# Kernel optimization log

Measured on AMD Instinct MI355X. Metric: run time of the kernel, lower is better.

Reference implementation:

```python
import jax, jax.numpy as jnp
import numpy as np

RADIUS = 4
SIGMA_1 = 5.0
SIGMA_2 = 1.0


def _gaussian_kernel(dtype):
    # norm.pdf(d)/norm.pdf(0) == exp(-d^2/2)
    x2 = jnp.linspace(-RADIUS, RADIUS, 2 * RADIUS + 1) ** 2
    dist = jnp.sqrt(x2[:, None] + x2[None, :]) / SIGMA_1
    return jnp.exp(-0.5 * dist ** 2).astype(dtype)  # [k, k]


def setup_inputs() -> dict:
    key = jax.random.key(0)
    k1, k2 = jax.random.split(key)
    labels = jax.random.uniform(k1, (16, 20, 256, 256), dtype=jnp.float32)
    inputs = jax.random.uniform(k2, (16, 3, 256, 256), dtype=jnp.float32)
    return {"labels": labels, "inputs": inputs}


def reference(labels, inputs):
    B, K, H, W = labels.shape
    kernel = _gaussian_kernel(labels.dtype)

    # per-class mean color: mean(inputs * probs, HW) / (mean(probs, HW) + 1e-5)
    pmean = jnp.mean(labels, axis=(2, 3))                           # [B, K]
    xmean = jnp.einsum('bchw,bkhw->bkc', inputs, labels) / (H * W)  # [B, K, C]
    class_mean = xmean / (pmean[..., None] + 1e-5)                  # [B, K, C]

    # diff = sum_c (x_c - m_c)^2, expanded to avoid a [B,K,C,H,W] intermediate
    x2sum = jnp.sum(inputs ** 2, axis=1)                            # [B, H, W]
    cross = jnp.einsum('bchw,bkc->bkhw', inputs, class_mean)        # [B, K, H, W]
    m2 = jnp.sum(class_mean ** 2, axis=-1)                          # [B, K]
    diff = x2sum[:, None] - 2.0 * cross + m2[:, :, None, None]      # [B, K, H, W]
    weights = jnp.exp(-(diff ** 2) / (SIGMA_2 ** 2))                # [B, K, H, W]

    def blur(x):  # single-channel gaussian conv, vectorized over B*K
        lhs = x.reshape(B * K, 1, H, W)
        rhs = kernel[None, None]  # [1, 1, k, k]
        y = jax.lax.conv_general_dilated(
            lhs, rhs, window_strides=(1, 1),
            padding=[(RADIUS, RADIUS), (RADIUS, RADIUS)],
            dimension_numbers=('NCHW', 'OIHW', 'NCHW'))
        return y.reshape(B, K, H, W)

    num = jnp.sum(labels * blur(labels * weights), axis=(0, 2, 3))  # [K]
    den = jnp.sum(labels * blur(weights), axis=(0, 2, 3))           # [K]
    loss = jnp.sum(jnp.abs(num / (den + 1e-6)))
    return jnp.asarray(K, labels.dtype) - loss
```

## Files before the change

### kernel.cpp

```cpp
#include <hip/hip_runtime.h>

#define B_ 16
#define K_ 20
#define H_ 256
#define W_ 256
#define HW_ (H_*W_)
#define BK_ (B_*K_)
#define TH_ 64
#define BATCH_ 8
#define KT_ 5
#define SCH_ 16
#define NBLK_FUSED_ (4*K_*B_)

#define WS_ND_   (SCH_*4*BK_)
#define WS_CNT_  (WS_ND_ + 2*NBLK_FUSED_)

#define G1T 0.980198673f
#define G2T 0.923116346f
#define G3T 0.835270211f
#define G4T 0.726149037f

__device__ __forceinline__ float rfl(float v) {
    return __int_as_float(__builtin_amdgcn_readfirstlane(__float_as_int(v)));
}

__global__ __launch_bounds__(256) void stats_k(const float* __restrict__ labels,
                                               const float* __restrict__ inputs,
                                               float* __restrict__ ws) {
    const int x = threadIdx.x;
    const int chunk = blockIdx.x;
    const int kt = blockIdx.y;
    const int b  = blockIdx.z;
    const int k0 = kt * KT_;
    if (chunk == 0 && kt == 0 && b == 0 && x == 0)
        ((unsigned*)(ws + WS_CNT_))[0] = 0u;

    const int cbase = chunk * (16 * W_ / 4);
    const float4* in0 = (const float4*)inputs + (size_t)b * 3 * (HW_/4) + cbase;
    const float4* in1 = in0 + (HW_/4);
    const float4* in2 = in1 + (HW_/4);
    const float4* lb  = (const float4*)labels + (size_t)(b * K_ + k0) * (HW_/4) + cbase;

    float acc[KT_][4];
#pragma unroll
    for (int kk = 0; kk < KT_; ++kk)
        acc[kk][0] = acc[kk][1] = acc[kk][2] = acc[kk][3] = 0.f;

#pragma unroll
    for (int it = 0; it < 4; ++it) {
        const int idx = it * 256 + x;
        const float4 a0 = in0[idx];
        const float4 a1 = in1[idx];
        const float4 a2 = in2[idx];
        float4 lv[KT_];
#pragma unroll
        for (int kk = 0; kk < KT_; ++kk) lv[kk] = lb[kk * (HW_/4) + idx];
#pragma unroll
        for (int kk = 0; kk < KT_; ++kk) {
            const float4 l = lv[kk];
            acc[kk][0] += (l.x + l.y) + (l.z + l.w);
            acc[kk][1] += fmaf(l.w, a0.w, fmaf(l.z, a0.z, fmaf(l.y, a0.y, l.x * a0.x)));
            acc[kk][2] += fmaf(l.w, a1.w, fmaf(l.z, a1.z, fmaf(l.y, a1.y, l.x * a1.x)));
            acc[kk][3] += fmaf(l.w, a2.w, fmaf(l.z, a2.z, fmaf(l.y, a2.y, l.x * a2.x)));
        }
    }

#pragma unroll
    for (int kk = 0; kk < KT_; ++kk)
#pragma unroll
        for (int q = 0; q < 4; ++q)
            for (int o = 32; o > 0; o >>= 1)
                acc[kk][q] += __shfl_down(acc[kk][q], o);

    __shared__ float sred[4][KT_][4];
    const int widx = x >> 6, lane = x & 63;
    if (lane == 0)
#pragma unroll
        for (int kk = 0; kk < KT_; ++kk)
#pragma unroll
            for (int q = 0; q < 4; ++q) sred[widx][kk][q] = acc[kk][q];
    __syncthreads();
    if (x < KT_ * 4) {
        const int kk = x >> 2, q = x & 3;
        const float v = sred[0][kk][q] + sred[1][kk][q] + sred[2][kk][q] + sred[3][kk][q];
        ws[(chunk * 4 + q) * BK_ + b * K_ + k0 + kk] = v;
    }
}

#define CAT(m) (((m) < 8) ? ring[(m)&7] : PL[(m)&7])

__global__ __launch_bounds__(256) void fused_k(const float* __restrict__ labels,
                                               const float* __restrict__ inputs,
                                               float* __restrict__ ws,
                                               float* __restrict__ out) {
    const int x = threadIdx.x;
    const int bid = blockIdx.x;
    const int swz = (bid & 7) * (NBLK_FUSED_ / 8) + (bid >> 3);
    const int b   = swz / (4 * K_);
    const int rem = swz - b * (4 * K_);
    const int k   = rem >> 2;
    const int sg  = rem & 3;
    const int bk  = b * K_ + k;
    const int r0  = sg * TH_;

    float s0 = 0.f, s1 = 0.f, s2 = 0.f, s3 = 0.f;
#pragma unroll
    for (int c = 0; c < SCH_; ++c) {
        const float* p = ws + c * 4 * BK_;
        s0 += p[bk]; s1 += p[BK_ + bk]; s2 += p[2*BK_ + bk]; s3 += p[3*BK_ + bk];
    }
    const float dnv = s0 + 1e-5f * (float)HW_;
    const float c0 = s1 / dnv, c1 = s2 / dnv, c2 = s3 / dnv;
    const float tc0 = rfl(2.f * c0), tc1 = rfl(2.f * c1), tc2 = rfl(2.f * c2);
    const float m2v = rfl(c0*c0 + c1*c1 + c2*c2);

    const float* lb  = labels + (size_t)bk * HW_;
    const float* i0p = inputs + (size_t)b * 3 * HW_;
    const float* i1p = i0p + HW_;
    const float* i2p = i1p + HW_;

    __shared__ float sv[2][BATCH_][W_ + 8];
    if (x < 128) {
        const int bu = x >> 6, j = (x >> 3) & 7, p = x & 7;
        const int col = (p < 4) ? p : (W_ + p);
        sv[bu][j][col] = 0.f;
    }

    float ring[8], PL[8], PW[8];
#pragma unroll
    for (int i = 0; i < 8; ++i) {
        const int gr = r0 - 4 + i;
        ring[i] = (gr >= 0) ? lb[gr * W_ + x] : 0.f;
    }
#pragma unroll
    for (int i = 0; i < 8; ++i)
        PL[i] = lb[(r0 + 4 + i) * W_ + x];
#pragma unroll
    for (int i = 0; i < 8; ++i) {
        const int r = r0 + i;
        const float a0 = i0p[r * W_ + x], a1 = i1p[r * W_ + x], a2 = i2p[r * W_ + x];
        const float d = fmaf(a0, a0 - tc0, fmaf(a1, a1 - tc1, fmaf(a2, a2 - tc2, m2v)));
        PW[i] = __expf(-d * d);
    }
    __syncthreads();

    float num = 0.f, den = 0.f;
#pragma unroll 1
    for (int bt = 0; bt < TH_ / BATCH_; ++bt) {
        const int R = r0 + bt * BATCH_;
        const int bf = bt & 1;
        float NL[8];
#pragma unroll
        for (int i = 0; i < 8; ++i) {
            const int gr = R + 12 + i;
            NL[i] = (gr < H_) ? lb[gr * W_ + x] : 0.f;
        }
        float a0v[8], a1v[8], a2v[8];
#pragma unroll
        for (int i = 0; i < 8; ++i) {
            int r = R + 8 + i; r = (r < H_) ? r : H_ - 1;
            a0v[i] = i0p[r * W_ + x]; a1v[i] = i1p[r * W_ + x]; a2v[i] = i2p[r * W_ + x];
        }
#pragma unroll
        for (int j = 0; j < 8; ++j) {
            const float v = fmaf(G4T, CAT(j) + CAT(j+8),
                            fmaf(G3T, CAT(j+1) + CAT(j+7),
                            fmaf(G2T, CAT(j+2) + CAT(j+6),
                            fmaf(G1T, CAT(j+3) + CAT(j+5), CAT(j+4)))));
            sv[bf][j][4 + x] = v;
        }
        asm volatile("s_waitcnt lgkmcnt(0)" ::: "memory");
        __builtin_amdgcn_s_barrier();
        asm volatile("" ::: "memory");
#pragma unroll
        for (int j = 0; j < 8; ++j) {
            const float* s = &sv[bf][j][x];
            const float bl = fmaf(G4T, s[0] + s[8],
                             fmaf(G3T, s[1] + s[7],
                             fmaf(G2T, s[2] + s[6],
                             fmaf(G1T, s[3] + s[5], s[4]))));
            const float t = PW[j] * bl;
            den += t;
            num = fmaf(CAT(j+4), t, num);
        }
#pragma unroll
        for (int i = 0; i < 8; ++i) {
            const float d = fmaf(a0v[i], a0v[i] - tc0,
                            fmaf(a1v[i], a1v[i] - tc1,
                            fmaf(a2v[i], a2v[i] - tc2, m2v)));
            const float w = __expf(-d * d);
            ring[i] = PL[i]; PL[i] = NL[i]; PW[i] = w;
        }
    }

    const int widx = x >> 6, lane = x & 63;
    for (int o = 32; o > 0; o >>= 1) { num += __shfl_down(num, o); den += __shfl_down(den, o); }
    __shared__ float rb[4][2];
    __shared__ unsigned sdone;
    __syncthreads();
    if (lane == 0) { rb[widx][0] = num; rb[widx][1] = den; }
    __syncthreads();
    if (x == 0) {
        const float fn = rb[0][0] + rb[1][0] + rb[2][0] + rb[3][0];
        const float fd = rb[0][1] + rb[1][1] + rb[2][1] + rb[3][1];
        float2* nd2 = (float2*)(ws + WS_ND_);
        nd2[k * 64 + b * 4 + sg] = make_float2(fn, fd);
        __threadfence();
        sdone = atomicAdd((unsigned*)(ws + WS_CNT_), 1u);
    }
    __syncthreads();
    if (sdone == (unsigned)(NBLK_FUSED_ - 1)) {
        __threadfence();
        if (x < 64) {
            float term = 0.f;
            if (x < K_) {
                const float2* nd2 = (const float2*)(ws + WS_ND_);
                float ns = 0.f, ds = 0.f;
                for (int i = 0; i < 64; ++i) {
                    const float2 v = nd2[x * 64 + i];
                    ns += v.x; ds += v.y;
                }
                term = fabsf(ns / (ds + 1e-6f));
            }
            for (int o = 32; o > 0; o >>= 1) term += __shfl_down(term, o);
            if (x == 0) out[0] = (float)K_ - term;
        }
    }
}

extern "C" void kernel_launch(void* const* d_in, const int* in_sizes, int n_in,
                              void* d_out, int out_size, void* d_ws, size_t ws_size,
                              hipStream_t stream) {
    const float* labels = (const float*)d_in[0];
    const float* inputs = (const float*)d_in[1];
    float* ws = (float*)d_ws;

    stats_k<<<dim3(SCH_, K_ / KT_, B_), 256, 0, stream>>>(labels, inputs, ws);
    fused_k<<<NBLK_FUSED_, 256, 0, stream>>>(labels, inputs, ws, (float*)d_out);
}
```

Baseline: 197.0 us.

## Fuse class-statistics pass into main kernel with per-(b,k) spin barrier

Removes the separate statistics kernel. Each fused block now computes partial label sums and label-weighted color sums over its own 64-row slab, publishes them, and spins on a per-(b,k) arrival counter until all four slabs have reported. A tiny zero kernel resets the counters. The aim is to read each block's label slab while it is still hot in cache and to drop one full pass over labels. The cost is an inter-block spin wait, which assumes all four sibling blocks are co-resident and risks deadlock or stalls if they are not.

After: 294.3 us. 1.49x slower.

```diff
diff --git a/kernel.cpp b/kernel.cpp
--- a/kernel.cpp
+++ b/kernel.cpp
@@ -8,12 +8,11 @@
 #define BK_ (B_*K_)
 #define TH_ 64
 #define BATCH_ 8
-#define KT_ 5
-#define SCH_ 16
 #define NBLK_FUSED_ (4*K_*B_)
 
-#define WS_ND_   (SCH_*4*BK_)
-#define WS_CNT_  (WS_ND_ + 2*NBLK_FUSED_)
+#define WS_ND_   (16*BK_)
+#define WS_ARR_  (WS_ND_ + 2*NBLK_FUSED_)
+#define WS_CNT_  (WS_ARR_ + BK_)
 
 #define G1T 0.980198673f
 #define G2T 0.923116346f
@@ -24,67 +23,9 @@
     return __int_as_float(__builtin_amdgcn_readfirstlane(__float_as_int(v)));
 }
 
-__global__ __launch_bounds__(256) void stats_k(const float* __restrict__ labels,
-                                               const float* __restrict__ inputs,
-                                               float* __restrict__ ws) {
-    const int x = threadIdx.x;
-    const int chunk = blockIdx.x;
-    const int kt = blockIdx.y;
-    const int b  = blockIdx.z;
-    const int k0 = kt * KT_;
-    if (chunk == 0 && kt == 0 && b == 0 && x == 0)
-        ((unsigned*)(ws + WS_CNT_))[0] = 0u;
-
-    const int cbase = chunk * (16 * W_ / 4);
-    const float4* in0 = (const float4*)inputs + (size_t)b * 3 * (HW_/4) + cbase;
-    const float4* in1 = in0 + (HW_/4);
-    const float4* in2 = in1 + (HW_/4);
-    const float4* lb  = (const float4*)labels + (size_t)(b * K_ + k0) * (HW_/4) + cbase;
-
-    float acc[KT_][4];
-#pragma unroll
-    for (int kk = 0; kk < KT_; ++kk)
-        acc[kk][0] = acc[kk][1] = acc[kk][2] = acc[kk][3] = 0.f;
-
-#pragma unroll
-    for (int it = 0; it < 4; ++it) {
-        const int idx = it * 256 + x;
-        const float4 a0 = in0[idx];
-        const float4 a1 = in1[idx];
-        const float4 a2 = in2[idx];
-        float4 lv[KT_];
-#pragma unroll
-        for (int kk = 0; kk < KT_; ++kk) lv[kk] = lb[kk * (HW_/4) + idx];
-#pragma unroll
-        for (int kk = 0; kk < KT_; ++kk) {
-            const float4 l = lv[kk];
-            acc[kk][0] += (l.x + l.y) + (l.z + l.w);
-            acc[kk][1] += fmaf(l.w, a0.w, fmaf(l.z, a0.z, fmaf(l.y, a0.y, l.x * a0.x)));
-            acc[kk][2] += fmaf(l.w, a1.w, fmaf(l.z, a1.z, fmaf(l.y, a1.y, l.x * a1.x)));
-            acc[kk][3] += fmaf(l.w, a2.w, fmaf(l.z, a2.z, fmaf(l.y, a2.y, l.x * a2.x)));
-        }
-    }
-
-#pragma unroll
-    for (int kk = 0; kk < KT_; ++kk)
-#pragma unroll
-        for (int q = 0; q < 4; ++q)
-            for (int o = 32; o > 0; o >>= 1)
-                acc[kk][q] += __shfl_down(acc[kk][q], o);
-
-    __shared__ float sred[4][KT_][4];
-    const int widx = x >> 6, lane = x & 63;
-    if (lane == 0)
-#pragma unroll
-        for (int kk = 0; kk < KT_; ++kk)
-#pragma unroll
-            for (int q = 0; q < 4; ++q) sred[widx][kk][q] = acc[kk][q];
-    __syncthreads();
-    if (x < KT_ * 4) {
-        const int kk = x >> 2, q = x & 3;
-        const float v = sred[0][kk][q] + sred[1][kk][q] + sred[2][kk][q] + sred[3][kk][q];
-        ws[(chunk * 4 + q) * BK_ + b * K_ + k0 + kk] = v;
-    }
+__global__ __launch_bounds__(256) void zero_k(float* ws) {
+    const int i = blockIdx.x * 256 + threadIdx.x;
+    if (i < BK_ + 1) ((unsigned*)(ws + WS_ARR_))[i] = 0u;
 }
 
 #define CAT(m) (((m) < 8) ? ring[(m)&7] : PL[(m)&7])
@@ -94,6 +35,7 @@
                                                float* __restrict__ ws,
                                                float* __restrict__ out) {
     const int x = threadIdx.x;
+    const int lane = x & 63, widx = x >> 6;
     const int bid = blockIdx.x;
     const int swz = (bid & 7) * (NBLK_FUSED_ / 8) + (bid >> 3);
     const int b   = swz / (4 * K_);
@@ -103,28 +45,71 @@
     const int bk  = b * K_ + k;
     const int r0  = sg * TH_;
 
+    const float* lb  = labels + (size_t)bk * HW_;
+    const float* i0p = inputs + (size_t)b * 3 * HW_;
+    const float* i1p = i0p + HW_;
+    const float* i2p = i1p + HW_;
+
+    __shared__ float sv[2][BATCH_][W_ + 8];
+    __shared__ float sred[4][4];
+    if (x < 128) {
+        const int bu = x >> 6, j = (x >> 3) & 7, p = x & 7;
+        const int col = (p < 4) ? p : (W_ + p);
+        sv[bu][j][col] = 0.f;
+    }
+
+    {
+        const float4* l4 = (const float4*)lb  + r0 * (W_/4);
+        const float4* p0 = (const float4*)i0p + r0 * (W_/4);
+        const float4* p1 = (const float4*)i1p + r0 * (W_/4);
+        const float4* p2 = (const float4*)i2p + r0 * (W_/4);
+        float4 aL = make_float4(0.f,0.f,0.f,0.f), a0 = aL, a1 = aL, a2 = aL;
+#pragma unroll 2
+        for (int it = 0; it < (TH_ * W_ / 4) / 256; ++it) {
+            const int idx = it * 256 + x;
+            const float4 l = l4[idx];
+            const float4 q0 = p0[idx];
+            const float4 q1 = p1[idx];
+            const float4 q2 = p2[idx];
+            aL.x += l.x; aL.y += l.y; aL.z += l.z; aL.w += l.w;
+            a0.x = fmaf(l.x,q0.x,a0.x); a0.y = fmaf(l.y,q0.y,a0.y);
+            a0.z = fmaf(l.z,q0.z,a0.z); a0.w = fmaf(l.w,q0.w,a0.w);
+            a1.x = fmaf(l.x,q1.x,a1.x); a1.y = fmaf(l.y,q1.y,a1.y);
+            a1.z = fmaf(l.z,q1.z,a1.z); a1.w = fmaf(l.w,q1.w,a1.w);
+            a2.x = fmaf(l.x,q2.x,a2.x); a2.y = fmaf(l.y,q2.y,a2.y);
+            a2.z = fmaf(l.z,q2.z,a2.z); a2.w = fmaf(l.w,q2.w,a2.w);
+        }
+        float v[4] = {(aL.x+aL.y)+(aL.z+aL.w), (a0.x+a0.y)+(a0.z+a0.w),
+                      (a1.x+a1.y)+(a1.z+a1.w), (a2.x+a2.y)+(a2.z+a2.w)};
+#pragma unroll
+        for (int q = 0; q < 4; ++q)
+            for (int o = 32; o > 0; o >>= 1) v[q] += __shfl_down(v[q], o);
+        if (lane == 0) { sred[widx][0]=v[0]; sred[widx][1]=v[1]; sred[widx][2]=v[2]; sred[widx][3]=v[3]; }
+        __syncthreads();
+        if (x == 0) {
+#pragma unroll
+            for (int q = 0; q < 4; ++q)
+                ws[(sg * 4 + q) * BK_ + bk] =
+                    sred[0][q] + sred[1][q] + sred[2][q] + sred[3][q];
+            __threadfence();
+            atomicAdd((int*)(ws + WS_ARR_) + bk, 1);
+            int* arr = (int*)(ws + WS_ARR_) + bk;
+            while (__hip_atomic_load(arr, __ATOMIC_ACQUIRE, __HIP_MEMORY_SCOPE_AGENT) < 4)
+                __builtin_amdgcn_s_sleep(2);
+        }
+        __syncthreads();
+    }
+
     float s0 = 0.f, s1 = 0.f, s2 = 0.f, s3 = 0.f;
 #pragma unroll
-    for (int c = 0; c < SCH_; ++c) {
-        const float* p = ws + c * 4 * BK_;
-        s0 += p[bk]; s1 += p[BK_ + bk]; s2 += p[2*BK_ + bk]; s3 += p[3*BK_ + bk];
+    for (int g = 0; g < 4; ++g) {
+        s0 += ws[(g*4+0)*BK_ + bk]; s1 += ws[(g*4+1)*BK_ + bk];
+        s2 += ws[(g*4+2)*BK_ + bk]; s3 += ws[(g*4+3)*BK_ + bk];
     }
     const float dnv = s0 + 1e-5f * (float)HW_;
     const float c0 = s1 / dnv, c1 = s2 / dnv, c2 = s3 / dnv;
     const float tc0 = rfl(2.f * c0), tc1 = rfl(2.f * c1), tc2 = rfl(2.f * c2);
     const float m2v = rfl(c0*c0 + c1*c1 + c2*c2);
-
-    const float* lb  = labels + (size_t)bk * HW_;
-    const float* i0p = inputs + (size_t)b * 3 * HW_;
-    const float* i1p = i0p + HW_;
-    const float* i2p = i1p + HW_;
-
-    __shared__ float sv[2][BATCH_][W_ + 8];
-    if (x < 128) {
-        const int bu = x >> 6, j = (x >> 3) & 7, p = x & 7;
-        const int col = (p < 4) ? p : (W_ + p);
-        sv[bu][j][col] = 0.f;
-    }
 
     float ring[8], PL[8], PW[8];
 #pragma unroll
@@ -193,7 +178,6 @@
         }
     }
 
-    const int widx = x >> 6, lane = x & 63;
     for (int o = 32; o > 0; o >>= 1) { num += __shfl_down(num, o); den += __shfl_down(den, o); }
     __shared__ float rb[4][2];
     __shared__ unsigned sdone;
@@ -235,6 +219,6 @@
     const float* inputs = (const float*)d_in[1];
     float* ws = (float*)d_ws;
 
-    stats_k<<<dim3(SCH_, K_ / KT_, B_), 256, 0, stream>>>(labels, inputs, ws);
+    zero_k<<<2, 256, 0, stream>>>(ws);
     fused_k<<<NBLK_FUSED_, 256, 0, stream>>>(labels, inputs, ws, (float*)d_out);
 }
```

## Process two classes per block, sharing input loads, with shorter row strips

Applied to the files above, without the earlier changes.

Each fused block now handles a pair of classes over a 32-row strip instead of one class over 64 rows. The input-colour loads and the x² sum are shared by both classes, and the weights are computed inline from stored distances. The shared buffer no longer double-buffers by iteration, so a second barrier per batch is added. The grid stays the same size, with more halo overhead per strip and higher register pressure in exchange for fewer redundant input reads.

New measurement: 204.5 us. +3.8%, slower.

```diff
diff --git a/kernel.cpp b/kernel.cpp
--- a/kernel.cpp
+++ b/kernel.cpp
@@ -6,14 +6,16 @@
 #define W_ 256
 #define HW_ (H_*W_)
 #define BK_ (B_*K_)
-#define TH_ 64
+#define TH_ 32
 #define BATCH_ 8
 #define KT_ 5
 #define SCH_ 16
-#define NBLK_FUSED_ (4*K_*B_)
+#define NSTR_ 8
+#define NKP_ 10
+#define NBLK_FUSED_ (NSTR_*NKP_*B_)
 
 #define WS_ND_   (SCH_*4*BK_)
-#define WS_CNT_  (WS_ND_ + 2*NBLK_FUSED_)
+#define WS_CNT_  (WS_ND_ + 2*K_*B_*NSTR_)
 
 #define G1T 0.980198673f
 #define G2T 0.923116346f
@@ -87,73 +89,87 @@
     }
 }
 
-#define CAT(m) (((m) < 8) ? ring[(m)&7] : PL[(m)&7])
+#define CAT0(m) (((m) < 8) ? ring0[(m)&7] : PL0[(m)&7])
+#define CAT1(m) (((m) < 8) ? ring1[(m)&7] : PL1[(m)&7])
 
 __global__ __launch_bounds__(256) void fused_k(const float* __restrict__ labels,
                                                const float* __restrict__ inputs,
                                                float* __restrict__ ws,
                                                float* __restrict__ out) {
     const int x = threadIdx.x;
+    const int lane = x & 63, widx = x >> 6;
     const int bid = blockIdx.x;
     const int swz = (bid & 7) * (NBLK_FUSED_ / 8) + (bid >> 3);
-    const int b   = swz / (4 * K_);
-    const int rem = swz - b * (4 * K_);
-    const int k   = rem >> 2;
-    const int sg  = rem & 3;
-    const int bk  = b * K_ + k;
+    const int b   = swz / (NSTR_ * NKP_);
+    const int rem = swz - b * (NSTR_ * NKP_);
+    const int kp  = rem >> 3;
+    const int sg  = rem & 7;
+    const int bk0 = b * K_ + kp * 2;
     const int r0  = sg * TH_;
 
-    float s0 = 0.f, s1 = 0.f, s2 = 0.f, s3 = 0.f;
-#pragma unroll
-    for (int c = 0; c < SCH_; ++c) {
-        const float* p = ws + c * 4 * BK_;
-        s0 += p[bk]; s1 += p[BK_ + bk]; s2 += p[2*BK_ + bk]; s3 += p[3*BK_ + bk];
-    }
-    const float dnv = s0 + 1e-5f * (float)HW_;
-    const float c0 = s1 / dnv, c1 = s2 / dnv, c2 = s3 / dnv;
-    const float tc0 = rfl(2.f * c0), tc1 = rfl(2.f * c1), tc2 = rfl(2.f * c2);
-    const float m2v = rfl(c0*c0 + c1*c1 + c2*c2);
-
-    const float* lb  = labels + (size_t)bk * HW_;
+    float tcx[2], tcy[2], tcz[2], m2a[2];
+#pragma unroll
+    for (int kk = 0; kk < 2; ++kk) {
+        float s0 = 0.f, s1 = 0.f, s2 = 0.f, s3 = 0.f;
+#pragma unroll
+        for (int c = 0; c < SCH_; ++c) {
+            const float* p = ws + c * 4 * BK_;
+            s0 += p[bk0+kk]; s1 += p[BK_ + bk0+kk];
+            s2 += p[2*BK_ + bk0+kk]; s3 += p[3*BK_ + bk0+kk];
+        }
+        const float dnv = s0 + 1e-5f * (float)HW_;
+        const float c0 = s1 / dnv, c1 = s2 / dnv, c2 = s3 / dnv;
+        tcx[kk] = rfl(2.f * c0); tcy[kk] = rfl(2.f * c1); tcz[kk] = rfl(2.f * c2);
+        m2a[kk] = rfl(c0*c0 + c1*c1 + c2*c2);
+    }
+
+    const float* lb0 = labels + (size_t)bk0 * HW_;
+    const float* lb1 = lb0 + HW_;
     const float* i0p = inputs + (size_t)b * 3 * HW_;
     const float* i1p = i0p + HW_;
     const float* i2p = i1p + HW_;
 
     __shared__ float sv[2][BATCH_][W_ + 8];
     if (x < 128) {
-        const int bu = x >> 6, j = (x >> 3) & 7, p = x & 7;
+        const int kk = x >> 6, j = (x >> 3) & 7, p = x & 7;
         const int col = (p < 4) ? p : (W_ + p);
-        sv[bu][j][col] = 0.f;
-    }
-
-    float ring[8], PL[8], PW[8];
+        sv[kk][j][col] = 0.f;
+    }
+
+    float ring0[8], ring1[8], PL0[8], PL1[8], dv[2][8];
 #pragma unroll
     for (int i = 0; i < 8; ++i) {
         const int gr = r0 - 4 + i;
-        ring[i] = (gr >= 0) ? lb[gr * W_ + x] : 0.f;
-    }
-#pragma unroll
-    for (int i = 0; i < 8; ++i)
-        PL[i] = lb[(r0 + 4 + i) * W_ + x];
+        ring0[i] = (gr >= 0) ? lb0[gr * W_ + x] : 0.f;
+        ring1[i] = (gr >= 0) ? lb1[gr * W_ + x] : 0.f;
+    }
+#pragma unroll
+    for (int i = 0; i < 8; ++i) {
+        PL0[i] = lb0[(r0 + 4 + i) * W_ + x];
+        PL1[i] = lb1[(r0 + 4 + i) * W_ + x];
+    }
 #pragma unroll
     for (int i = 0; i < 8; ++i) {
         const int r = r0 + i;
         const float a0 = i0p[r * W_ + x], a1 = i1p[r * W_ + x], a2 = i2p[r * W_ + x];
-        const float d = fmaf(a0, a0 - tc0, fmaf(a1, a1 - tc1, fmaf(a2, a2 - tc2, m2v)));
-        PW[i] = __expf(-d * d);
-    }
-    __syncthreads();
-
-    float num = 0.f, den = 0.f;
+        const float x2 = fmaf(a0, a0, fmaf(a1, a1, a2 * a2));
+#pragma unroll
+        for (int kk = 0; kk < 2; ++kk)
+            dv[kk][i] = fmaf(-a0, tcx[kk], fmaf(-a1, tcy[kk], fmaf(-a2, tcz[kk], x2 + m2a[kk])));
+    }
+    __syncthreads();
+
+    float num0 = 0.f, den0 = 0.f, num1 = 0.f, den1 = 0.f;
 #pragma unroll 1
     for (int bt = 0; bt < TH_ / BATCH_; ++bt) {
         const int R = r0 + bt * BATCH_;
-        const int bf = bt & 1;
-        float NL[8];
+        float NL0[8], NL1[8];
 #pragma unroll
         for (int i = 0; i < 8; ++i) {
             const int gr = R + 12 + i;
-            NL[i] = (gr < H_) ? lb[gr * W_ + x] : 0.f;
+            const bool in = (gr < H_);
+            NL0[i] = in ? lb0[gr * W_ + x] : 0.f;
+            NL1[i] = in ? lb1[gr * W_ + x] : 0.f;
         }
         float a0v[8], a1v[8], a2v[8];
 #pragma unroll
@@ -163,48 +179,69 @@
         }
 #pragma unroll
         for (int j = 0; j < 8; ++j) {
-            const float v = fmaf(G4T, CAT(j) + CAT(j+8),
-                            fmaf(G3T, CAT(j+1) + CAT(j+7),
-                            fmaf(G2T, CAT(j+2) + CAT(j+6),
-                            fmaf(G1T, CAT(j+3) + CAT(j+5), CAT(j+4)))));
-            sv[bf][j][4 + x] = v;
+            sv[0][j][4 + x] = fmaf(G4T, CAT0(j) + CAT0(j+8),
+                              fmaf(G3T, CAT0(j+1) + CAT0(j+7),
+                              fmaf(G2T, CAT0(j+2) + CAT0(j+6),
+                              fmaf(G1T, CAT0(j+3) + CAT0(j+5), CAT0(j+4)))));
+            sv[1][j][4 + x] = fmaf(G4T, CAT1(j) + CAT1(j+8),
+                              fmaf(G3T, CAT1(j+1) + CAT1(j+7),
+                              fmaf(G2T, CAT1(j+2) + CAT1(j+6),
+                              fmaf(G1T, CAT1(j+3) + CAT1(j+5), CAT1(j+4)))));
         }
         asm volatile("s_waitcnt lgkmcnt(0)" ::: "memory");
         __builtin_amdgcn_s_barrier();
         asm volatile("" ::: "memory");
 #pragma unroll
         for (int j = 0; j < 8; ++j) {
-            const float* s = &sv[bf][j][x];
-            const float bl = fmaf(G4T, s[0] + s[8],
-                             fmaf(G3T, s[1] + s[7],
-                             fmaf(G2T, s[2] + s[6],
-                             fmaf(G1T, s[3] + s[5], s[4]))));
-            const float t = PW[j] * bl;
-            den += t;
-            num = fmaf(CAT(j+4), t, num);
-        }
+            const float* s0p = &sv[0][j][x];
+            const float bl0 = fmaf(G4T, s0p[0] + s0p[8],
+                              fmaf(G3T, s0p[1] + s0p[7],
+                              fmaf(G2T, s0p[2] + s0p[6],
+                              fmaf(G1T, s0p[3] + s0p[5], s0p[4]))));
+            const float* s1p = &sv[1][j][x];
+            const float bl1 = fmaf(G4T, s1p[0] + s1p[8],
+                              fmaf(G3T, s1p[1] + s1p[7],
+                              fmaf(G2T, s1p[2] + s1p[6],
+                              fmaf(G1T, s1p[3] + s1p[5], s1p[4]))));
+            const float w0 = __expf(-dv[0][j] * dv[0][j]);
+            const float w1 = __expf(-dv[1][j] * dv[1][j]);
+            const float t0 = w0 * bl0;
+            const float t1 = w1 * bl1;
+            den0 += t0; den1 += t1;
+            num0 = fmaf(CAT0(j+4), t0, num0);
+            num1 = fmaf(CAT1(j+4), t1, num1);
+        }
+        __builtin_amdgcn_s_barrier();
+        asm volatile("" ::: "memory");
 #pragma unroll
         for (int i = 0; i < 8; ++i) {
-            const float d = fmaf(a0v[i], a0v[i] - tc0,
-                            fmaf(a1v[i], a1v[i] - tc1,
-                            fmaf(a2v[i], a2v[i] - tc2, m2v)));
-            const float w = __expf(-d * d);
-            ring[i] = PL[i]; PL[i] = NL[i]; PW[i] = w;
-        }
-    }
-
-    const int widx = x >> 6, lane = x & 63;
-    for (int o = 32; o > 0; o >>= 1) { num += __shfl_down(num, o); den += __shfl_down(den, o); }
-    __shared__ float rb[4][2];
+            const float a0 = a0v[i], a1 = a1v[i], a2 = a2v[i];
+            const float x2 = fmaf(a0, a0, fmaf(a1, a1, a2 * a2));
+            dv[0][i] = fmaf(-a0, tcx[0], fmaf(-a1, tcy[0], fmaf(-a2, tcz[0], x2 + m2a[0])));
+            dv[1][i] = fmaf(-a0, tcx[1], fmaf(-a1, tcy[1], fmaf(-a2, tcz[1], x2 + m2a[1])));
+            ring0[i] = PL0[i]; PL0[i] = NL0[i];
+            ring1[i] = PL1[i]; PL1[i] = NL1[i];
+        }
+    }
+
+    for (int o = 32; o > 0; o >>= 1) {
+        num0 += __shfl_down(num0, o); den0 += __shfl_down(den0, o);
+        num1 += __shfl_down(num1, o); den1 += __shfl_down(den1, o);
+    }
+    __shared__ float rb[4][4];
     __shared__ unsigned sdone;
     __syncthreads();
-    if (lane == 0) { rb[widx][0] = num; rb[widx][1] = den; }
+    if (lane == 0) { rb[widx][0] = num0; rb[widx][1] = den0; rb[widx][2] = num1; rb[widx][3] = den1; }
     __syncthreads();
     if (x == 0) {
-        const float fn = rb[0][0] + rb[1][0] + rb[2][0] + rb[3][0];
-        const float fd = rb[0][1] + rb[1][1] + rb[2][1] + rb[3][1];
         float2* nd2 = (float2*)(ws + WS_ND_);
-        nd2[k * 64 + b * 4 + sg] = make_float2(fn, fd);
+        const int base = b * NSTR_ + sg;
+        nd2[(kp*2    ) * (B_*NSTR_) + base] =
+            make_float2(rb[0][0]+rb[1][0]+rb[2][0]+rb[3][0],
+                        rb[0][1]+rb[1][1]+rb[2][1]+rb[3][1]);
+        nd2[(kp*2 + 1) * (B_*NSTR_) + base] =
+            make_float2(rb[0][2]+rb[1][2]+rb[2][2]+rb[3][2],
+                        rb[0][3]+rb[1][3]+rb[2][3]+rb[3][3]);
         __threadfence();
         sdone = atomicAdd((unsigned*)(ws + WS_CNT_), 1u);
     }
@@ -216,8 +253,8 @@
             if (x < K_) {
                 const float2* nd2 = (const float2*)(ws + WS_ND_);
                 float ns = 0.f, ds = 0.f;
-                for (int i = 0; i < 64; ++i) {
-                    const float2 v = nd2[x * 64 + i];
+                for (int i = 0; i < B_*NSTR_; ++i) {
+                    const float2 v = nd2[x * (B_*NSTR_) + i];
                     ns += v.x; ds += v.y;
                 }
                 term = fabsf(ns / (ds + 1e-6f));
```

## Pack row pairs into float2 shared buffer and widen stats class tile

Applied to the files above, without the earlier changes.

The fused kernel's shared-memory staging buffer now stores two vertically blurred rows per float2 element, so the horizontal blur pass reads half as many LDS entries using 64-bit accesses. The stats kernel processes ten classes per block instead of five and loads each label vector inside the accumulate loop, which halves the number of times the inputs are re-read. The larger class tile raises register pressure in the stats kernel, and float2 LDS accesses may change bank-conflict behaviour.

After: 203.0 us. 3.1% more time.

```diff
diff --git a/kernel.cpp b/kernel.cpp
--- a/kernel.cpp
+++ b/kernel.cpp
@@ -8,7 +8,7 @@
 #define BK_ (B_*K_)
 #define TH_ 64
 #define BATCH_ 8
-#define KT_ 5
+#define KT_ 10
 #define SCH_ 16
 #define NBLK_FUSED_ (4*K_*B_)
 
@@ -52,12 +52,9 @@
         const float4 a0 = in0[idx];
         const float4 a1 = in1[idx];
         const float4 a2 = in2[idx];
-        float4 lv[KT_];
-#pragma unroll
-        for (int kk = 0; kk < KT_; ++kk) lv[kk] = lb[kk * (HW_/4) + idx];
 #pragma unroll
         for (int kk = 0; kk < KT_; ++kk) {
-            const float4 l = lv[kk];
+            const float4 l = lb[kk * (HW_/4) + idx];
             acc[kk][0] += (l.x + l.y) + (l.z + l.w);
             acc[kk][1] += fmaf(l.w, a0.w, fmaf(l.z, a0.z, fmaf(l.y, a0.y, l.x * a0.x)));
             acc[kk][2] += fmaf(l.w, a1.w, fmaf(l.z, a1.z, fmaf(l.y, a1.y, l.x * a1.x)));
@@ -119,11 +116,11 @@
     const float* i1p = i0p + HW_;
     const float* i2p = i1p + HW_;
 
-    __shared__ float sv[2][BATCH_][W_ + 8];
-    if (x < 128) {
-        const int bu = x >> 6, j = (x >> 3) & 7, p = x & 7;
+    __shared__ float2 sv[2][BATCH_/2][W_ + 8];
+    if (x < 64) {
+        const int bu = x >> 5, j2 = (x >> 3) & 3, p = x & 7;
         const int col = (p < 4) ? p : (W_ + p);
-        sv[bu][j][col] = 0.f;
+        sv[bu][j2][col] = make_float2(0.f, 0.f);
     }
 
     float ring[8], PL[8], PW[8];
@@ -162,26 +159,39 @@
             a0v[i] = i0p[r * W_ + x]; a1v[i] = i1p[r * W_ + x]; a2v[i] = i2p[r * W_ + x];
         }
 #pragma unroll
-        for (int j = 0; j < 8; ++j) {
-            const float v = fmaf(G4T, CAT(j) + CAT(j+8),
-                            fmaf(G3T, CAT(j+1) + CAT(j+7),
-                            fmaf(G2T, CAT(j+2) + CAT(j+6),
-                            fmaf(G1T, CAT(j+3) + CAT(j+5), CAT(j+4)))));
-            sv[bf][j][4 + x] = v;
+        for (int j2 = 0; j2 < 4; ++j2) {
+            const int j = 2 * j2;
+            const float v0 = fmaf(G4T, CAT(j) + CAT(j+8),
+                             fmaf(G3T, CAT(j+1) + CAT(j+7),
+                             fmaf(G2T, CAT(j+2) + CAT(j+6),
+                             fmaf(G1T, CAT(j+3) + CAT(j+5), CAT(j+4)))));
+            const float v1 = fmaf(G4T, CAT(j+1) + CAT(j+9),
+                             fmaf(G3T, CAT(j+2) + CAT(j+8),
+                             fmaf(G2T, CAT(j+3) + CAT(j+7),
+                             fmaf(G1T, CAT(j+4) + CAT(j+6), CAT(j+5)))));
+            sv[bf][j2][4 + x] = make_float2(v0, v1);
         }
         asm volatile("s_waitcnt lgkmcnt(0)" ::: "memory");
         __builtin_amdgcn_s_barrier();
         asm volatile("" ::: "memory");
 #pragma unroll
-        for (int j = 0; j < 8; ++j) {
-            const float* s = &sv[bf][j][x];
-            const float bl = fmaf(G4T, s[0] + s[8],
-                             fmaf(G3T, s[1] + s[7],
-                             fmaf(G2T, s[2] + s[6],
-                             fmaf(G1T, s[3] + s[5], s[4]))));
-            const float t = PW[j] * bl;
-            den += t;
-            num = fmaf(CAT(j+4), t, num);
+        for (int j2 = 0; j2 < 4; ++j2) {
+            const int j = 2 * j2;
+            const float2* s = &sv[bf][j2][x];
+            const float2 t0 = s[0], t1 = s[1], t2 = s[2], t3 = s[3], t4 = s[4],
+                         t5 = s[5], t6 = s[6], t7 = s[7], t8 = s[8];
+            const float blx = fmaf(G4T, t0.x + t8.x,
+                              fmaf(G3T, t1.x + t7.x,
+                              fmaf(G2T, t2.x + t6.x,
+                              fmaf(G1T, t3.x + t5.x, t4.x))));
+            const float bly = fmaf(G4T, t0.y + t8.y,
+                              fmaf(G3T, t1.y + t7.y,
+                              fmaf(G2T, t2.y + t6.y,
+                              fmaf(G1T, t3.y + t5.y, t4.y))));
+            const float u0 = PW[j]   * blx;
+            const float u1 = PW[j+1] * bly;
+            den += u0 + u1;
+            num = fmaf(CAT(j+4), u0, fmaf(CAT(j+5), u1, num));
         }
 #pragma unroll
         for (int i = 0; i < 8; ++i) {
```
